# Performance work log

Measured on AMD Instinct MI355X. Metric: run time of the kernel, lower is better.

## Reference

```python
import jax, jax.numpy as jnp
import numpy as np


def _conv3(x, w):
    # 3x3 conv, stride 1, padding 1 (SAME), NCHW/OIHW
    return jax.lax.conv_general_dilated(
        x, w, window_strides=(1, 1), padding=((1, 1), (1, 1)),
        dimension_numbers=("NCHW", "OIHW", "NCHW"))


def setup_inputs() -> dict:
    key = jax.random.key(0)
    ks = jax.random.split(key, 10)
    B, C, H, W = 16, 64, 128, 128
    NL = 4
    inp = {
        "x0": jax.random.normal(ks[0], (B, C, H, W), dtype=jnp.float32),
        "spa_mask": jax.random.uniform(ks[1], (B, 1, H, W), dtype=jnp.float32),
        # uniform noise in (0,1) for gumbel; bounded away from 0 like the torch retry loop
        "gumbels": jax.random.uniform(ks[2], (1, C, NL, 2), dtype=jnp.float32,
                                      minval=1e-6, maxval=1.0 - 1e-6),
        "ch_mask_param": jax.random.uniform(ks[3], (1, C, NL, 2), dtype=jnp.float32),
        "w0": jax.random.normal(ks[4], (C, C, 3, 3), dtype=jnp.float32) * 0.05,
        "w1": jax.random.normal(ks[5], (C, C, 3, 3), dtype=jnp.float32) * 0.05,
        "w2": jax.random.normal(ks[6], (C, C, 3, 3), dtype=jnp.float32) * 0.05,
        "w3": jax.random.normal(ks[7], (C, C, 3, 3), dtype=jnp.float32) * 0.05,
        "wc": jax.random.normal(ks[8], (C, C * NL, 1, 1), dtype=jnp.float32) * 0.05,
        "bc": jax.random.normal(ks[9], (C,), dtype=jnp.float32) * 0.05,
    }
    return inp


def reference(x0, spa_mask, gumbels, ch_mask_param, w0, w1, w2, w3, wc, bc):
    tau = 1.0
    g = -jnp.log(-jnp.log(gumbels))
    ch_mask = jax.nn.softmax((ch_mask_param + g) / tau, axis=3)  # (1,C,NL,2)
    ws = [w0, w1, w2, w3]
    outs = []
    fea = x0
    for i in range(4):
        m_d = ch_mask[:, :, i, 0][:, :, None, None]  # dense-path channel gate (1,C,1,1)
        m_s = ch_mask[:, :, i, 1][:, :, None, None]  # sparse-path channel gate
        if i == 0:
            fea = _conv3(fea, ws[0])
            fea = fea * m_s * spa_mask + fea * m_d
        else:
            fea_d = _conv3(fea * m_d, ws[i])
            fea_s = _conv3(fea * m_s, ws[i])
            fea = (fea_d * m_s * spa_mask + fea_d * m_d
                   + fea_s * m_s * spa_mask + fea_s * m_d * spa_mask)
        fea = jax.nn.relu(fea)
        outs.append(fea)
    cat = jnp.concatenate(outs, axis=1)  # (B, 4C, H, W)
    out = jnp.einsum("oc,bchw->bohw", wc[:, :, 0, 0], cat) + bc[None, :, None, None]
    return (out, ch_mask)
```

## Files before the change

### kernel.cpp

```cpp
#include <hip/hip_runtime.h>
#include <math.h>

#define B_ 16
#define C_ 64
#define H_ 128
#define W_ 128
#define HW_ (H_*W_)
#define OUT_ELEMS 16777216

#define CHM_B    0
#define PWA_B    2048
#define AH_B     34816
#define FEA_B(s) (550912u + (size_t)(s)*33554432u)

#define A_S0   0
#define A_S(s) (36864 + ((s)-1)*73728)

typedef __attribute__((ext_vector_type(4))) short  v4s;
typedef __attribute__((ext_vector_type(8))) short  v8s;
typedef __attribute__((ext_vector_type(4))) float  v4f;

__device__ __forceinline__ ushort f2bf(float f) {
    unsigned u = __builtin_bit_cast(unsigned, f);
    unsigned r = u + 0x7FFFu + ((u >> 16) & 1u);
    return (ushort)(r >> 16);
}
__device__ __forceinline__ v8s ld_b64x2(const ushort* p) {
    v4s a = *(const v4s*)(const void*)p;
    v4s b = *(const v4s*)(const void*)(p + 4);
    return __builtin_shufflevector(a, b, 0, 1, 2, 3, 4, 5, 6, 7);
}

__global__ __launch_bounds__(64) void mask_kernel(
    const float* __restrict__ gum, const float* __restrict__ par,
    float* __restrict__ chm, float* __restrict__ out_tail)
{
    int c = threadIdx.x;
    #pragma unroll
    for (int i = 0; i < 4; ++i) {
        int base = (c*4 + i)*2;
        float g0 = -logf(-logf(gum[base]));
        float g1 = -logf(-logf(gum[base+1]));
        float a0 = par[base] + g0, a1 = par[base+1] + g1;
        float mx = fmaxf(a0, a1);
        float e0 = expf(a0 - mx), e1 = expf(a1 - mx);
        float inv = 1.0f / (e0 + e1);
        float m0 = e0*inv, m1 = e1*inv;
        chm[base] = m0; chm[base+1] = m1;
        out_tail[base] = m0; out_tail[base+1] = m1;
    }
}

__global__ __launch_bounds__(256) void prep_kernel(
    const float* __restrict__ w0, const float* __restrict__ w1,
    const float* __restrict__ w2, const float* __restrict__ w3,
    const float* __restrict__ wc, const float* __restrict__ chm,
    ushort* __restrict__ AH, ushort* __restrict__ pwA)
{
    int idx = blockIdx.x*256 + threadIdx.x;
    if (idx < 36864) {
        int blk = idx >> 11;
        int r3  = idx & 2047;
        int oc = r3 >> 5, icl = r3 & 31;
        int cc = blk / 9, t = blk - 9*cc;
        int ic = cc*32 + icl;
        AH[idx] = f2bf(w0[(oc*64 + ic)*9 + t]);
    } else if (idx < 258048) {
        int j = idx - 36864;
        int s = 1 + j / 73728;
        int r = j % 73728;
        int blk = r >> 12;
        int r3  = r & 4095;
        int ocM = r3 >> 5, icl = r3 & 31;
        int cc = blk / 9, t = blk - 9*cc;
        int ic = cc*32 + icl;
        int oc = ocM >> 1, set = ocM & 1;
        const float* wsrc = (s == 1) ? w1 : (s == 2 ? w2 : w3);
        AH[idx] = f2bf(wsrc[(oc*64 + ic)*9 + t] * chm[(ic*4 + s)*2 + set]);
    } else {
        int r = idx - 258048;
        pwA[r] = f2bf(wc[r]);
    }
}

template<int NSETS, bool INF32>
__global__ __launch_bounds__(256, 2) void conv_bf16(
    const void* __restrict__ inv, const ushort* __restrict__ A,
    const float* __restrict__ chm, const float* __restrict__ spa,
    ushort* __restrict__ feaOut, int stage)
{
    constexpr int MOC = 64*NSETS;
    constexpr int MT  = MOC/32;
    __shared__ __align__(16) ushort sB[3*130*36];

    const int tid  = threadIdx.x;
    const int lane = tid & 63, wave = tid >> 6;
    const int wrow = wave >> 1, wcol = wave & 1;
    const int q = lane >> 4, ln16 = lane & 15;
    const int wk = (blockIdx.x & 7)*256 + (blockIdx.x >> 3);
    const int h = wk & 127, b = wk >> 7;

    {
        v8s z = (v8s){0,0,0,0,0,0,0,0};
        for (int e = tid; e < 1755; e += 256)
            *(v8s*)(void*)(sB + e*8) = z;
    }

    v4f acc[MT][4];
    #pragma unroll
    for (int m = 0; m < MT; ++m)
        #pragma unroll
        for (int n = 0; n < 4; ++n) acc[m][n] = (v4f){0.f, 0.f, 0.f, 0.f};

    int aRow[MT];
    #pragma unroll
    for (int m = 0; m < MT; ++m)
        aRow[m] = (wrow*(MOC/2) + m*16 + ln16)*32 + q*8;

    v8s stgA[6], stgB[6];
    v4f stgAF[12], stgBF[12];

    auto issue = [&](int ic0, v8s* stg, v4f* stgF) {
        #pragma unroll
        for (int it = 0; it < 6; ++it) {
            int i  = it*256 + tid;
            int ry = i >> 9;
            int r  = i & 511;
            int ic = r >> 4, wv = r & 15;
            int gh = h - 1 + ry;
            if constexpr (INF32) {
                v4f a0 = (v4f){0.f,0.f,0.f,0.f}, a1 = a0;
                if ((unsigned)gh < 128u) {
                    const float* s = (const float*)inv +
                        ((size_t)((b*C_ + ic0 + ic)*H_ + gh)*W_ + wv*8);
                    a0 = *(const v4f*)(const void*)s;
                    a1 = *(const v4f*)(const void*)(s + 4);
                }
                stgF[it*2] = a0; stgF[it*2+1] = a1;
            } else {
                v8s v = (v8s){0,0,0,0,0,0,0,0};
                if ((unsigned)gh < 128u)
                    v = *(const v8s*)(const void*)((const ushort*)inv +
                        ((size_t)((b*C_ + ic0 + ic)*H_ + gh)*W_ + wv*8));
                stg[it] = v;
            }
        }
    };
    auto scatter = [&](const v8s* stg, const v4f* stgF) {
        #pragma unroll
        for (int it = 0; it < 6; ++it) {
            int i  = it*256 + tid;
            int ry = i >> 9;
            int r  = i & 511;
            int ic = r >> 4, wv = r & 15;
            int colBase = ry*130 + wv*8 + 1;
            ushort vals[8];
            if constexpr (INF32) {
                #pragma unroll
                for (int j = 0; j < 4; ++j) {
                    vals[j]   = f2bf(stgF[it*2][j]);
                    vals[4+j] = f2bf(stgF[it*2+1][j]);
                }
            } else {
                #pragma unroll
                for (int j = 0; j < 8; ++j) vals[j] = (ushort)stg[it][j];
            }
            #pragma unroll
            for (int j = 0; j < 8; ++j) {
                int colIdx = colBase + j;
                sB[colIdx*36 + (ic ^ (((colIdx >> 3) & 3) << 3))] = vals[j];
            }
        }
    };
    auto compute = [&](const ushort* Ab) {
        v8s af0[MT], af1[MT], af2[MT];
        #pragma unroll
        for (int m = 0; m < MT; ++m)
            af0[m] = *(const v8s*)(const void*)(Ab + aRow[m]);
        #pragma unroll
        for (int m = 0; m < MT; ++m)
            af1[m] = *(const v8s*)(const void*)(Ab + MOC*32 + aRow[m]);
        #pragma unroll
        for (int t = 0; t < 9; ++t) {
            if (t < 7) {
                #pragma unroll
                for (int m = 0; m < MT; ++m)
                    af2[m] = *(const v8s*)(const void*)(Ab + (t+2)*MOC*32 + aRow[m]);
            }
            const int ky = t/3, kx = t - 3*(t/3);
            #pragma unroll
            for (int nt = 0; nt < 4; ++nt) {
                int colIdx = ky*130 + wcol*64 + nt*16 + ln16 + kx;
                v8s bf = ld_b64x2(&sB[colIdx*36 + ((q ^ ((colIdx >> 3) & 3)) << 3)]);
                #pragma unroll
                for (int m = 0; m < MT; ++m)
                    acc[m][nt] = __builtin_amdgcn_mfma_f32_16x16x32_bf16(af0[m], bf, acc[m][nt], 0, 0, 0);
            }
            #pragma unroll
            for (int m = 0; m < MT; ++m) { af0[m] = af1[m]; af1[m] = af2[m]; }
        }
    };

    issue(0, stgA, stgAF);
    __syncthreads();
    scatter(stgA, stgAF);
    issue(32, stgB, stgBF);
    __syncthreads();
    compute(A);
    __syncthreads();
    scatter(stgB, stgBF);
    __syncthreads();
    compute(A + 9*MOC*32);

    const float* spaRow = &spa[b*HW_ + h*W_];
    #pragma unroll
    for (int nt = 0; nt < 4; ++nt) {
        int px = wcol*64 + nt*16 + ln16;
        float sp = spaRow[px];
        #pragma unroll
        for (int m = 0; m < MT; ++m) {
            if constexpr (NSETS == 2) {
                #pragma unroll
                for (int rp = 0; rp < 2; ++rp) {
                    int oc = wrow*32 + m*8 + q*2 + rp;
                    float md = chm[(oc*4 + stage)*2 + 0];
                    float ms = chm[(oc*4 + stage)*2 + 1];
                    float f = acc[m][nt][2*rp]*(ms*sp + md)
                            + acc[m][nt][2*rp+1]*((ms + md)*sp);
                    feaOut[((size_t)(b*C_ + oc)*H_ + h)*W_ + px] = f2bf(fmaxf(f, 0.f));
                }
            } else {
                #pragma unroll
                for (int r = 0; r < 4; ++r) {
                    int oc = wrow*32 + m*16 + q*4 + r;
                    float md = chm[(oc*4 + stage)*2 + 0];
                    float ms = chm[(oc*4 + stage)*2 + 1];
                    float f = acc[m][nt][r]*(ms*sp + md);
                    feaOut[((size_t)(b*C_ + oc)*H_ + h)*W_ + px] = f2bf(fmaxf(f, 0.f));
                }
            }
        }
    }
}

__global__ __launch_bounds__(256, 2) void pw_final(
    const ushort* __restrict__ fea, const ushort* __restrict__ pwA,
    const float* __restrict__ bc, float* __restrict__ out)
{
    __shared__ __align__(16) ushort sF[64*260];

    const int tid  = threadIdx.x;
    const int lane = tid & 63, wave = tid >> 6;
    const int wrow = wave >> 1, wcol = wave & 1;
    const int q = lane >> 4, ln16 = lane & 15;
    const int half = blockIdx.x & 1;
    const int h = (blockIdx.x >> 1) & 127;
    const int b = blockIdx.x >> 8;
    const int px0 = half*64;

    {
        v8s stg[8];
        #pragma unroll
        for (int it = 0; it < 8; ++it) {
            int i  = it*256 + tid;
            int s  = i >> 9;
            int r  = i & 511;
            int ic = r >> 3, pxv = r & 7;
            stg[it] = *(const v8s*)(const void*)(
                fea + (size_t)s*OUT_ELEMS + ((size_t)(b*C_ + ic)*H_ + h)*W_ + px0 + pxv*8);
        }
        #pragma unroll
        for (int it = 0; it < 8; ++it) {
            int i  = it*256 + tid;
            int s  = i >> 9;
            int r  = i & 511;
            int ic = r >> 3, pxv = r & 7;
            int kS = (s*64 + ic) ^ ((pxv & 3) << 3);
            ushort* dst = &sF[(pxv*8)*260 + kS];
            #pragma unroll
            for (int j = 0; j < 8; ++j) dst[j*260] = (ushort)stg[it][j];
        }
    }
    __syncthreads();

    v4f acc[2][2];
    #pragma unroll
    for (int m = 0; m < 2; ++m)
        #pragma unroll
        for (int n = 0; n < 2; ++n) acc[m][n] = (v4f){0.f, 0.f, 0.f, 0.f};

    #pragma unroll
    for (int ks = 0; ks < 8; ++ks) {
        v8s a[2];
        #pragma unroll
        for (int m = 0; m < 2; ++m)
            a[m] = *(const v8s*)(const void*)(pwA + (wrow*32 + m*16 + ln16)*256 + ks*32 + q*8);
        #pragma unroll
        for (int n = 0; n < 2; ++n) {
            int px = wcol*32 + n*16 + ln16;
            int swz = (px >> 3) & 3;
            v8s bf = ld_b64x2(&sF[px*260 + ks*32 + ((q ^ swz) << 3)]);
            #pragma unroll
            for (int m = 0; m < 2; ++m)
                acc[m][n] = __builtin_amdgcn_mfma_f32_16x16x32_bf16(a[m], bf, acc[m][n], 0, 0, 0);
        }
    }

    #pragma unroll
    for (int n = 0; n < 2; ++n) {
        int px = px0 + wcol*32 + n*16 + ln16;
        #pragma unroll
        for (int m = 0; m < 2; ++m)
            #pragma unroll
            for (int r = 0; r < 4; ++r) {
                int o = wrow*32 + m*16 + q*4 + r;
                out[((size_t)(b*C_ + o)*H_ + h)*W_ + px] = acc[m][n][r] + bc[o];
            }
    }
}

extern "C" void kernel_launch(void* const* d_in, const int* in_sizes, int n_in,
                              void* d_out, int out_size, void* d_ws, size_t ws_size,
                              hipStream_t stream)
{
    const float* x0  = (const float*)d_in[0];
    const float* spa = (const float*)d_in[1];
    const float* gum = (const float*)d_in[2];
    const float* par = (const float*)d_in[3];
    const float* w0  = (const float*)d_in[4];
    const float* w1  = (const float*)d_in[5];
    const float* w2  = (const float*)d_in[6];
    const float* w3  = (const float*)d_in[7];
    const float* wc  = (const float*)d_in[8];
    const float* bc  = (const float*)d_in[9];
    float* out = (float*)d_out;
    char*  ws  = (char*)d_ws;

    float*  chm = (float*)(ws + CHM_B);
    ushort* pwA = (ushort*)(ws + PWA_B);
    ushort* AH  = (ushort*)(ws + AH_B);
    ushort* fea0 = (ushort*)(ws + FEA_B(0));
    ushort* fea1 = (ushort*)(ws + FEA_B(1));
    ushort* fea2 = (ushort*)(ws + FEA_B(2));
    ushort* fea3 = (ushort*)(ws + FEA_B(3));

    mask_kernel<<<1, 64, 0, stream>>>(gum, par, chm, out + OUT_ELEMS);
    prep_kernel<<<1072, 256, 0, stream>>>(w0, w1, w2, w3, wc, chm, AH, pwA);

    conv_bf16<1, true ><<<2048, 256, 0, stream>>>(x0,   AH + A_S0,  chm, spa, fea0, 0);
    conv_bf16<2, false><<<2048, 256, 0, stream>>>(fea0, AH + A_S(1), chm, spa, fea1, 1);
    conv_bf16<2, false><<<2048, 256, 0, stream>>>(fea1, AH + A_S(2), chm, spa, fea2, 2);
    conv_bf16<2, false><<<2048, 256, 0, stream>>>(fea2, AH + A_S(3), chm, spa, fea3, 3);

    pw_final<<<4096, 256, 0, stream>>>(fea0, pwA, bc, out);
}
```

Measured before the change: 426.8 us.

## Deepen conv weight prefetch, drop LDS zero-fill, refine swizzle and staging

The 3x3 conv kernel drops the full shared-memory zero-fill and zeroes only the padding columns. It also uses a single staging buffer instead of two and keeps a 4-deep ring of weight fragments, prefetched three taps ahead, with the next half's weights loaded before the barrier. The LDS swizzle changes to a 3-bit XOR pattern with half-swapped 64-bit reads, meant to reduce bank conflicts. Together these cut shared-memory stores and register pressure and hide weight-load latency, at the cost of more complex indexing and reliance on the scatter covering every non-pad slot.

New measurement: 417.7 us. 1.02x faster.

```diff
diff --git a/kernel.cpp b/kernel.cpp
--- a/kernel.cpp
+++ b/kernel.cpp
@@ -24,11 +24,6 @@
     unsigned u = __builtin_bit_cast(unsigned, f);
     unsigned r = u + 0x7FFFu + ((u >> 16) & 1u);
     return (ushort)(r >> 16);
-}
-__device__ __forceinline__ v8s ld_b64x2(const ushort* p) {
-    v4s a = *(const v4s*)(const void*)p;
-    v4s b = *(const v4s*)(const void*)(p + 4);
-    return __builtin_shufflevector(a, b, 0, 1, 2, 3, 4, 5, 6, 7);
 }
 
 __global__ __launch_bounds__(64) void mask_kernel(
@@ -100,12 +95,6 @@
     const int wk = (blockIdx.x & 7)*256 + (blockIdx.x >> 3);
     const int h = wk & 127, b = wk >> 7;
 
-    {
-        v8s z = (v8s){0,0,0,0,0,0,0,0};
-        for (int e = tid; e < 1755; e += 256)
-            *(v8s*)(void*)(sB + e*8) = z;
-    }
-
     v4f acc[MT][4];
     #pragma unroll
     for (int m = 0; m < MT; ++m)
@@ -117,10 +106,11 @@
     for (int m = 0; m < MT; ++m)
         aRow[m] = (wrow*(MOC/2) + m*16 + ln16)*32 + q*8;
 
-    v8s stgA[6], stgB[6];
-    v4f stgAF[12], stgBF[12];
-
-    auto issue = [&](int ic0, v8s* stg, v4f* stgF) {
+    v8s stg[6];
+    v4f stgF[12];
+    v8s af[4][MT];
+
+    auto issue = [&](int ic0) {
         #pragma unroll
         for (int it = 0; it < 6; ++it) {
             int i  = it*256 + tid;
@@ -146,7 +136,7 @@
             }
         }
     };
-    auto scatter = [&](const v8s* stg, const v4f* stgF) {
+    auto scatter = [&]() {
         #pragma unroll
         for (int it = 0; it < 6; ++it) {
             int i  = it*256 + tid;
@@ -168,47 +158,60 @@
             #pragma unroll
             for (int j = 0; j < 8; ++j) {
                 int colIdx = colBase + j;
-                sB[colIdx*36 + (ic ^ (((colIdx >> 3) & 3) << 3))] = vals[j];
-            }
-        }
+                int s3 = (colIdx >> 3) & 7;
+                sB[colIdx*36 + (ic ^ (s3 << 2))] = vals[j];
+            }
+        }
+    };
+    auto prolog = [&](const ushort* Ab) {
+        #pragma unroll
+        for (int tp = 0; tp < 3; ++tp)
+            #pragma unroll
+            for (int m = 0; m < MT; ++m)
+                af[tp][m] = *(const v8s*)(const void*)(Ab + tp*MOC*32 + aRow[m]);
     };
     auto compute = [&](const ushort* Ab) {
-        v8s af0[MT], af1[MT], af2[MT];
-        #pragma unroll
-        for (int m = 0; m < MT; ++m)
-            af0[m] = *(const v8s*)(const void*)(Ab + aRow[m]);
-        #pragma unroll
-        for (int m = 0; m < MT; ++m)
-            af1[m] = *(const v8s*)(const void*)(Ab + MOC*32 + aRow[m]);
         #pragma unroll
         for (int t = 0; t < 9; ++t) {
-            if (t < 7) {
+            if (t < 6) {
                 #pragma unroll
                 for (int m = 0; m < MT; ++m)
-                    af2[m] = *(const v8s*)(const void*)(Ab + (t+2)*MOC*32 + aRow[m]);
+                    af[(t+3)&3][m] = *(const v8s*)(const void*)(Ab + (t+3)*MOC*32 + aRow[m]);
             }
             const int ky = t/3, kx = t - 3*(t/3);
             #pragma unroll
             for (int nt = 0; nt < 4; ++nt) {
                 int colIdx = ky*130 + wcol*64 + nt*16 + ln16 + kx;
-                v8s bf = ld_b64x2(&sB[colIdx*36 + ((q ^ ((colIdx >> 3) & 3)) << 3)]);
+                int s3 = (colIdx >> 3) & 7;
+                int base = colIdx*36 + ((q ^ (s3 >> 1)) << 3);
+                int lo = base + ((s3 & 1) << 2);
+                int hi = base + (((s3 & 1) ^ 1) << 2);
+                v4s va = *(const v4s*)(const void*)(sB + lo);
+                v4s vb = *(const v4s*)(const void*)(sB + hi);
+                v8s bf = __builtin_shufflevector(va, vb, 0, 1, 2, 3, 4, 5, 6, 7);
                 #pragma unroll
                 for (int m = 0; m < MT; ++m)
-                    acc[m][nt] = __builtin_amdgcn_mfma_f32_16x16x32_bf16(af0[m], bf, acc[m][nt], 0, 0, 0);
-            }
-            #pragma unroll
-            for (int m = 0; m < MT; ++m) { af0[m] = af1[m]; af1[m] = af2[m]; }
+                    acc[m][nt] = __builtin_amdgcn_mfma_f32_16x16x32_bf16(af[t&3][m], bf, acc[m][nt], 0, 0, 0);
+            }
         }
     };
 
-    issue(0, stgA, stgAF);
-    __syncthreads();
-    scatter(stgA, stgAF);
-    issue(32, stgB, stgBF);
+    issue(0);
+    prolog(A);
+    if (tid < 216) {
+        int colSel = tid / 36;
+        int icz    = tid - colSel*36;
+        int ry     = colSel >> 1;
+        int colIdx = ry*130 + ((colSel & 1) ? 129 : 0);
+        sB[colIdx*36 + icz] = 0;
+    }
+    scatter();
+    issue(32);
     __syncthreads();
     compute(A);
+    prolog(A + 9*MOC*32);
     __syncthreads();
-    scatter(stgB, stgBF);
+    scatter();
     __syncthreads();
     compute(A + 9*MOC*32);
 
@@ -299,7 +302,9 @@
         for (int n = 0; n < 2; ++n) {
             int px = wcol*32 + n*16 + ln16;
             int swz = (px >> 3) & 3;
-            v8s bf = ld_b64x2(&sF[px*260 + ks*32 + ((q ^ swz) << 3)]);
+            v4s va = *(const v4s*)(const void*)(sF + px*260 + ks*32 + ((q ^ swz) << 3));
+            v4s vb = *(const v4s*)(const void*)(sF + px*260 + ks*32 + ((q ^ swz) << 3) + 4);
+            v8s bf = __builtin_shufflevector(va, vb, 0, 1, 2, 3, 4, 5, 6, 7);
             #pragma unroll
             for (int m = 0; m < 2; ++m)
                 acc[m][n] = __builtin_amdgcn_mfma_f32_16x16x32_bf16(a[m], bf, acc[m][n], 0, 0, 0);
```
